# Optimization experiments

Hardware: AMD Instinct MI355X
Metric: run time of the kernel (lower is better)

## Reference

```python
import jax, jax.numpy as jnp
import numpy as np

K = 3
PAD = 1

def conv2d(x, w, b=None):
    # x: [B,C,H,W], w: [O,C,kh,kw], stride 1, padding 1
    y = jax.lax.conv_general_dilated(x, w, (1, 1), [(PAD, PAD), (PAD, PAD)],
                                     dimension_numbers=('NCHW', 'OIHW', 'NCHW'))
    if b is not None:
        y = y + b[None, :, None, None]
    return y

def deform_conv2d(x, offset, mask, w):
    # Faithful torchvision DeformConv2d (v2, stride=1, dilation=1, pad=1, no bias).
    # x: [B,C,H,W]; offset: [B,2*K*K,H,W] with (dy,dx) interleaved per kernel pt;
    # mask: [B,K*K,H,W]; w: [O,C,K,K]
    B, C, H, W = x.shape
    KK = K * K
    off = offset.reshape(B, KK, 2, H, W)
    offs_y, offs_x = off[:, :, 0], off[:, :, 1]           # [B,KK,H,W]
    ky = (jnp.arange(KK) // K).astype(jnp.float32) - PAD   # kernel row offsets
    kx = (jnp.arange(KK) % K).astype(jnp.float32) - PAD    # kernel col offsets
    py = offs_y + jnp.arange(H, dtype=jnp.float32)[None, None, :, None] + ky[None, :, None, None]
    px = offs_x + jnp.arange(W, dtype=jnp.float32)[None, None, None, :] + kx[None, :, None, None]
    y0f = jnp.floor(py); x0f = jnp.floor(px)
    wy = py - y0f; wx = px - x0f                           # bilinear fractions
    y0 = y0f.astype(jnp.int32); x0 = x0f.astype(jnp.int32)
    xf = x.reshape(B, C, H * W)

    def corner(yi, xi):
        valid = ((yi >= 0) & (yi < H) & (xi >= 0) & (xi < W)).astype(x.dtype)
        idx = jnp.clip(yi, 0, H - 1) * W + jnp.clip(xi, 0, W - 1)   # [B,KK,H,W]
        g = jax.vmap(lambda img, ix: img[:, ix])(xf, idx.reshape(B, KK * H * W))
        return g.reshape(B, C, KK, H, W) * valid[:, None]

    one = jnp.asarray(1.0, x.dtype)
    samp = (corner(y0, x0)         * ((one - wy) * (one - wx))[:, None]
          + corner(y0, x0 + 1)     * ((one - wy) * wx)[:, None]
          + corner(y0 + 1, x0)     * (wy * (one - wx))[:, None]
          + corner(y0 + 1, x0 + 1) * (wy * wx)[:, None])       # [B,C,KK,H,W]
    if mask is not None:
        samp = samp * mask[:, None]
    O = w.shape[0]
    return jnp.einsum('bckhw,ock->bohw', samp, w.reshape(O, C, KK))

def setup_inputs() -> dict:
    key = jax.random.key(0)
    ks = jax.random.split(key, 7)
    B, C, O, H, W = 4, 64, 64, 128, 128
    x = jax.random.normal(ks[0], (B, C, H, W), jnp.float32)
    ele = jax.random.normal(ks[1], (B, 1, H, W), jnp.float32)
    offset_w = jax.random.normal(ks[2], (2 * K * K, 1, 3, 3), jnp.float32) * 0.1
    offset_b = jnp.zeros((2 * K * K,), jnp.float32)
    mask_w = jax.random.normal(ks[3], (K * K, C, 3, 3), jnp.float32) * (1.0 / np.sqrt(C * 9))
    mask_b = jnp.zeros((K * K,), jnp.float32)
    deform_w = jax.random.normal(ks[4], (O, C, K, K), jnp.float32) * (1.0 / np.sqrt(C * 9))
    return {"x": x, "ele": ele, "offset_w": offset_w, "offset_b": offset_b,
            "mask_w": mask_w, "mask_b": mask_b, "deform_w": deform_w}

def reference(x, ele, offset_w, offset_b, mask_w, mask_b, deform_w):
    offset = conv2d(ele, offset_w, offset_b)                 # [B,18,H,W]
    mask = jax.nn.sigmoid(conv2d(x, mask_w, mask_b))         # [B,9,H,W]
    out = deform_conv2d(x, offset, mask, deform_w)           # [B,O,H,W]
    return jax.nn.relu(out)
```

## Files before the change

kernel.cpp:

```cpp
#include <hip/hip_runtime.h>
#include <hip/hip_bf16.h>
#include <hip/hip_fp16.h>

typedef _Float16 half8 __attribute__((ext_vector_type(8)));
typedef _Float16 half2v __attribute__((ext_vector_type(2)));
typedef float f32x4 __attribute__((ext_vector_type(4)));

#define B_ 4
#define C_ 64
#define O_ 64
#define H_ 128
#define W_ 128
#define HT 8
#define WT 16
#define HALO 3
#define RS 14
#define CS 22

__device__ __forceinline__ unsigned pkh(float lo, float hi) {
  half2v v = {(_Float16)lo, (_Float16)hi};
  return __builtin_bit_cast(unsigned, v);
}

__global__ void build_frags(const float* __restrict__ dw,
                            const float* __restrict__ mw,
                            _Float16* __restrict__ wsb) {
  int t = blockIdx.x * 256 + threadIdx.x;
  if (t < 36864) {
    int j = t & 7, lane = (t >> 3) & 63, ot = (t >> 9) & 3, s = t >> 11;
    int kk = s >> 1, ch = s & 1;
    int o = ot * 16 + (lane & 15);
    int c = ch * 32 + ((lane >> 4) << 3) + j;
    wsb[t] = (_Float16)dw[(o * 64 + c) * 9 + kk];
  } else if (t < 46080) {
    int t2 = t - 36864;
    int j = t2 & 7, lane = (t2 >> 3) & 63, s = t2 >> 9;
    int km = lane & 15;
    int c = (s & 1) * 32 + ((lane >> 4) << 3) + j;
    int tap = s >> 1;
    float v = (km < 9) ? mw[(km * 64 + c) * 9 + tap] : 0.0f;
    wsb[t] = (_Float16)v;
  }
}

__global__ __launch_bounds__(512, 4)
void deform_main(const float* __restrict__ x,
                 const float* __restrict__ ele,
                 const float* __restrict__ ow,
                 const float* __restrict__ ob,
                 const float* __restrict__ mb,
                 const _Float16* __restrict__ wsb,
                 float* __restrict__ out) {
  __shared__ uint4 xs4[RS * CS * 9];
  __shared__ uint4 dynbuf4[1152];
  _Float16* offl = (_Float16*)dynbuf4;
  uint2* cwb = (uint2*)((char*)dynbuf4 + 4608);
  unsigned* crc = (unsigned*)((char*)dynbuf4 + 4608 + 9216);
  f32x4* redbuf = (f32x4*)dynbuf4;

  const int tid = threadIdx.x;
  const int lane = tid & 63;
  const int wv = tid >> 6;
  const int pcl = lane & 15;
  const int lq = lane >> 4;

  const int bid = blockIdx.x;
  const int d = ((bid & 7) << 6) + (bid >> 3);
  const int b = d >> 7;
  const int t7 = d & 127;
  const int r0 = (t7 >> 3) * HT;
  const int c0 = (t7 & 7) * WT;

  float ev[9];
  {
    int tl = tid & 127;
    int pr = tl >> 4, pc = tl & 15;
    int h = r0 + pr, w = c0 + pc;
#pragma unroll
    for (int ty = 0; ty < 3; ++ty)
#pragma unroll
      for (int tx = 0; tx < 3; ++tx) {
        int gy = h - 1 + ty, gx = w - 1 + tx;
        float v = 0.0f;
        if ((unsigned)gy < 128u && (unsigned)gx < 128u)
          v = ele[b * (H_ * W_) + (gy << 7) + gx];
        ev[ty * 3 + tx] = v;
      }
  }

  {
    _Float16* xsb = (_Float16*)xs4;
    const int c2 = tid >> 4;
    const int pl = tid & 15;
    const float* xb0 = x + b * (C_ * H_ * W_) + (2 * c2) * (H_ * W_);
    const float* xb1 = xb0 + (H_ * W_);

    float2 va[11], vb[11];
#pragma unroll
    for (int k = 0; k < 11; ++k) {
      int it = pl + k * 16;
      int live = it < 168;
      int itc = live ? it : 167;
      int row = (itc * 5462) >> 16;
      int pc2 = itc - row * 12;
      int gy = r0 - HALO + row;
      int gx = c0 - 4 + 2 * pc2;
      float2 a = {0.0f, 0.0f}, bv2 = {0.0f, 0.0f};
      if (live && (unsigned)gy < 128u && (unsigned)gx < 127u) {
        int gi = (gy << 7) + gx;
        a = *(const float2*)(xb0 + gi);
        bv2 = *(const float2*)(xb1 + gi);
      }
      va[k] = a;
      vb[k] = bv2;
    }
#pragma unroll
    for (int k = 0; k < 11; ++k) {
      int it = pl + k * 16;
      if (it < 168) {
        int row = (it * 5462) >> 16;
        int pc2 = it - row * 12;
        int p = row * CS + 2 * pc2 - 1;
        if (pc2 > 0) {
          half2v h0 = {(_Float16)va[k].x, (_Float16)vb[k].x};
          *(half2v*)(xsb + p * 72 + 2 * c2) = h0;
        }
        if (pc2 < 11) {
          half2v h1 = {(_Float16)va[k].y, (_Float16)vb[k].y};
          *(half2v*)(xsb + (p + 1) * 72 + 2 * c2) = h1;
        }
      }
    }
  }

  if (tid < 128) {
#pragma unroll
    for (int ci = 0; ci < 18; ++ci) {
      float a = ob[ci];
#pragma unroll
      for (int tap = 0; tap < 9; ++tap) a += ev[tap] * ow[ci * 9 + tap];
      offl[tid * 18 + ci] = (_Float16)a;
    }
  }
  __syncthreads();

  {
    const half8* wfm8 = ((const half8*)wsb) + 4608;
    f32x4 macc = {0.f, 0.f, 0.f, 0.f};
#pragma unroll
    for (int s = 0; s < 18; ++s) {
      const int tap = s >> 1;
      const int chalf = s & 1;
      const int ty = tap / 3, tx = tap - ty * 3;
      half8 aw = wfm8[s * 64 + lane];
      const int csl = chalf * 4 + lq;
      int rc = (wv + (HALO - 1) + ty) * CS + (pcl + (HALO - 1) + tx);
      half8 xv = *(const half8*)(xs4 + rc * 9 + csl);
      macc = __builtin_amdgcn_mfma_f32_16x16x32_f16(aw, xv, macc, 0, 0, 0);
    }
    const int px = wv * 16 + pcl;
    const int h = r0 + wv, w = c0 + pcl;
#pragma unroll
    for (int r = 0; r < 4; ++r) {
      int kk = lq * 4 + r;
      if (kk < 9) {
        float a = macc[r] + mb[kk];
        float m = 1.0f / (1.0f + __expf(-a));
        int ky = kk / 3 - 1;
        int kx = kk - (kk / 3) * 3 - 1;
        half2v o2 = *(const half2v*)&offl[px * 18 + kk * 2];
        float py = (float)(h + ky) + (float)o2[0];
        float pxx = (float)(w + kx) + (float)o2[1];
        float fy = floorf(py), fx = floorf(pxx);
        float wy = py - fy, wx = pxx - fx;
        int iy = (int)fy - r0 + HALO;
        int ix = (int)fx - c0 + HALO;
        int vy0 = (unsigned)iy < (unsigned)RS;
        int vy1 = (unsigned)(iy + 1) < (unsigned)RS;
        int vx0 = (unsigned)ix < (unsigned)CS;
        int vx1 = (unsigned)(ix + 1) < (unsigned)CS;
        int cy0 = min(max(iy, 0), RS - 1), cy1 = min(max(iy + 1, 0), RS - 1);
        int cx0 = min(max(ix, 0), CS - 1), cx1 = min(max(ix + 1, 0), CS - 1);
        float wy0 = 1.0f - wy, wx0 = 1.0f - wx;
        float a00 = wy0 * wx0 * m * (float)(vy0 & vx0);
        float a01 = wy0 * wx * m * (float)(vy0 & vx1);
        float a10 = wy * wx0 * m * (float)(vy1 & vx0);
        float a11 = wy * wx * m * (float)(vy1 & vx1);
        int rc00 = cy0 * CS + cx0;
        int drow = (cy1 - cy0) * CS;
        int dcol = cx1 - cx0;
        uint2 cv;
        cv.x = pkh(a00, a01);
        cv.y = pkh(a10, a11);
        cwb[px * 9 + kk] = cv;
        crc[px * 9 + kk] =
            (unsigned)rc00 | ((unsigned)drow << 16) | ((unsigned)dcol << 24);
      }
    }
  }
  __syncthreads();

  const half8* wf8 = (const half8*)wsb;
  const int pxg = wv & 3;
  const int kh = wv >> 2;
  f32x4 acc[2][4];
#pragma unroll
  for (int pt = 0; pt < 2; ++pt)
#pragma unroll
    for (int ot = 0; ot < 4; ++ot) {
      f32x4 z = {0.f, 0.f, 0.f, 0.f};
      acc[pt][ot] = z;
    }

  const int pxA = pxg * 32 + pcl;
  const int pxB = pxA + 16;

#pragma unroll
  for (int s = 0; s < 9; ++s) {
    const int sidx = kh * 9 + s;
    const int kk = sidx >> 1;
    const int ch = sidx & 1;
    const int csl = ch * 4 + lq;
    half8 t[2];
#pragma unroll
    for (int pt = 0; pt < 2; ++pt) {
      const int px = pt ? pxB : pxA;
      uint2 cv = cwb[px * 9 + kk];
      unsigned rv = crc[px * 9 + kk];
      int rc00 = rv & 0xFFFF;
      int drow = (rv >> 16) & 0xFF;
      int dcol = rv >> 24;
      int rc01 = rc00 + dcol;
      int rc10 = rc00 + drow;
      int rc11 = rc10 + dcol;
      half2v c01 = __builtin_bit_cast(half2v, cv.x);
      half2v c23 = __builtin_bit_cast(half2v, cv.y);
      _Float16 a00 = c01[0], a01 = c01[1], a10 = c23[0], a11 = c23[1];
      half8 a00s = {a00, a00, a00, a00, a00, a00, a00, a00};
      half8 a01s = {a01, a01, a01, a01, a01, a01, a01, a01};
      half8 a10s = {a10, a10, a10, a10, a10, a10, a10, a10};
      half8 a11s = {a11, a11, a11, a11, a11, a11, a11, a11};
      half8 v00 = *(const half8*)(xs4 + rc00 * 9 + csl);
      half8 v01 = *(const half8*)(xs4 + rc01 * 9 + csl);
      half8 v10 = *(const half8*)(xs4 + rc10 * 9 + csl);
      half8 v11 = *(const half8*)(xs4 + rc11 * 9 + csl);
      t[pt] = v00 * a00s + v01 * a01s + v10 * a10s + v11 * a11s;
    }
#pragma unroll
    for (int ot = 0; ot < 4; ++ot) {
      half8 bw = wf8[(sidx * 4 + ot) * 64 + lane];
      acc[0][ot] = __builtin_amdgcn_mfma_f32_16x16x32_f16(bw, t[0], acc[0][ot], 0, 0, 0);
      acc[1][ot] = __builtin_amdgcn_mfma_f32_16x16x32_f16(bw, t[1], acc[1][ot], 0, 0, 0);
    }
  }

  __syncthreads();

#pragma unroll
  for (int pt = 0; pt < 2; ++pt) {
    if (kh == 1) {
#pragma unroll
      for (int ot = 0; ot < 4; ++ot)
        redbuf[((pxg * 4 + ot) * 4 + lq) * 16 + pcl] = acc[pt][ot];
    }
    __syncthreads();
    if (kh == 0) {
      const int px = pt ? pxB : pxA;
      const int h = r0 + (px >> 4);
      const int w = c0 + pcl;
#pragma unroll
      for (int ot = 0; ot < 4; ++ot) {
        f32x4 other = redbuf[((pxg * 4 + ot) * 4 + lq) * 16 + pcl];
#pragma unroll
        for (int r = 0; r < 4; ++r) {
          int o = ot * 16 + lq * 4 + r;
          float v = fmaxf(acc[pt][ot][r] + other[r], 0.0f);
          out[((b * O_ + o) << 14) + (h << 7) + w] = v;
        }
      }
    }
    __syncthreads();
  }
}

extern "C" void kernel_launch(void* const* d_in, const int* in_sizes, int n_in,
                              void* d_out, int out_size, void* d_ws, size_t ws_size,
                              hipStream_t stream) {
  const float* x   = (const float*)d_in[0];
  const float* ele = (const float*)d_in[1];
  const float* ow  = (const float*)d_in[2];
  const float* ob  = (const float*)d_in[3];
  const float* mw  = (const float*)d_in[4];
  const float* mb  = (const float*)d_in[5];
  const float* dw  = (const float*)d_in[6];
  _Float16* wsb = (_Float16*)d_ws;

  build_frags<<<180, 256, 0, stream>>>(dw, mw, wsb);
  deform_main<<<512, 512, 0, stream>>>(x, ele, ow, ob, mb, wsb,
                                       (float*)d_out);
}
```

Measured before the change: 30.36 us.

## Double block size to 1024 threads and split deform work per wave

Launches 1024-thread blocks, so each wave handles one 16-pixel tile and one channel half instead of two tiles. The sampling-coefficient computation is split out of the mask MFMA stage into a separate pass spread over all threads, with the mask staged in shared memory. The final reduction becomes a symmetric exchange in which each wave of a pair writes half the output channels, reusing the x tile buffer. The aim is more waves to hide LDS and MFMA latency, at the cost of an extra barrier, tighter register limits from launch_bounds(1024,8), and fewer loads per thread in the x staging.

```diff
diff --git a/kernel.cpp b/kernel.cpp
--- a/kernel.cpp
+++ b/kernel.cpp
@@ -43,7 +43,7 @@
   }
 }
 
-__global__ __launch_bounds__(512, 4)
+__global__ __launch_bounds__(1024, 8)
 void deform_main(const float* __restrict__ x,
                  const float* __restrict__ ele,
                  const float* __restrict__ ow,
@@ -52,11 +52,12 @@
                  const _Float16* __restrict__ wsb,
                  float* __restrict__ out) {
   __shared__ uint4 xs4[RS * CS * 9];
-  __shared__ uint4 dynbuf4[1152];
+  __shared__ uint4 dynbuf4[1296];
   _Float16* offl = (_Float16*)dynbuf4;
-  uint2* cwb = (uint2*)((char*)dynbuf4 + 4608);
-  unsigned* crc = (unsigned*)((char*)dynbuf4 + 4608 + 9216);
-  f32x4* redbuf = (f32x4*)dynbuf4;
+  _Float16* maskl = (_Float16*)((char*)dynbuf4 + 4608);
+  uint2* cwb = (uint2*)((char*)dynbuf4 + 4608 + 2304);
+  unsigned* crc = (unsigned*)((char*)dynbuf4 + 4608 + 2304 + 9216);
+  f32x4* xbuf = (f32x4*)xs4;
 
   const int tid = threadIdx.x;
   const int lane = tid & 63;
@@ -72,9 +73,8 @@
   const int c0 = (t7 & 7) * WT;
 
   float ev[9];
-  {
-    int tl = tid & 127;
-    int pr = tl >> 4, pc = tl & 15;
+  if (tid < 128) {
+    int pr = tid >> 4, pc = tid & 15;
     int h = r0 + pr, w = c0 + pc;
 #pragma unroll
     for (int ty = 0; ty < 3; ++ty)
@@ -90,15 +90,16 @@
 
   {
     _Float16* xsb = (_Float16*)xs4;
-    const int c2 = tid >> 4;
+    const int c2 = (tid >> 4) & 31;
     const int pl = tid & 15;
+    const int half = tid >> 9;
     const float* xb0 = x + b * (C_ * H_ * W_) + (2 * c2) * (H_ * W_);
     const float* xb1 = xb0 + (H_ * W_);
 
-    float2 va[11], vb[11];
-#pragma unroll
-    for (int k = 0; k < 11; ++k) {
-      int it = pl + k * 16;
+    float2 va[6], vb[6];
+#pragma unroll
+    for (int k = 0; k < 6; ++k) {
+      int it = pl + (2 * k + half) * 16;
       int live = it < 168;
       int itc = live ? it : 167;
       int row = (itc * 5462) >> 16;
@@ -115,8 +116,8 @@
       vb[k] = bv2;
     }
 #pragma unroll
-    for (int k = 0; k < 11; ++k) {
-      int it = pl + k * 16;
+    for (int k = 0; k < 6; ++k) {
+      int it = pl + (2 * k + half) * 16;
       if (it < 168) {
         int row = (it * 5462) >> 16;
         int pc2 = it - row * 12;
@@ -144,7 +145,7 @@
   }
   __syncthreads();
 
-  {
+  if (wv < 8) {
     const half8* wfm8 = ((const half8*)wsb) + 4608;
     f32x4 macc = {0.f, 0.f, 0.f, 0.f};
 #pragma unroll
@@ -158,62 +159,67 @@
       half8 xv = *(const half8*)(xs4 + rc * 9 + csl);
       macc = __builtin_amdgcn_mfma_f32_16x16x32_f16(aw, xv, macc, 0, 0, 0);
     }
-    const int px = wv * 16 + pcl;
-    const int h = r0 + wv, w = c0 + pcl;
+    int px = wv * 16 + pcl;
 #pragma unroll
     for (int r = 0; r < 4; ++r) {
-      int kk = lq * 4 + r;
-      if (kk < 9) {
-        float a = macc[r] + mb[kk];
+      int km = lq * 4 + r;
+      if (km < 9) {
+        float a = macc[r] + mb[km];
         float m = 1.0f / (1.0f + __expf(-a));
-        int ky = kk / 3 - 1;
-        int kx = kk - (kk / 3) * 3 - 1;
-        half2v o2 = *(const half2v*)&offl[px * 18 + kk * 2];
-        float py = (float)(h + ky) + (float)o2[0];
-        float pxx = (float)(w + kx) + (float)o2[1];
-        float fy = floorf(py), fx = floorf(pxx);
-        float wy = py - fy, wx = pxx - fx;
-        int iy = (int)fy - r0 + HALO;
-        int ix = (int)fx - c0 + HALO;
-        int vy0 = (unsigned)iy < (unsigned)RS;
-        int vy1 = (unsigned)(iy + 1) < (unsigned)RS;
-        int vx0 = (unsigned)ix < (unsigned)CS;
-        int vx1 = (unsigned)(ix + 1) < (unsigned)CS;
-        int cy0 = min(max(iy, 0), RS - 1), cy1 = min(max(iy + 1, 0), RS - 1);
-        int cx0 = min(max(ix, 0), CS - 1), cx1 = min(max(ix + 1, 0), CS - 1);
-        float wy0 = 1.0f - wy, wx0 = 1.0f - wx;
-        float a00 = wy0 * wx0 * m * (float)(vy0 & vx0);
-        float a01 = wy0 * wx * m * (float)(vy0 & vx1);
-        float a10 = wy * wx0 * m * (float)(vy1 & vx0);
-        float a11 = wy * wx * m * (float)(vy1 & vx1);
-        int rc00 = cy0 * CS + cx0;
-        int drow = (cy1 - cy0) * CS;
-        int dcol = cx1 - cx0;
-        uint2 cv;
-        cv.x = pkh(a00, a01);
-        cv.y = pkh(a10, a11);
-        cwb[px * 9 + kk] = cv;
-        crc[px * 9 + kk] =
-            (unsigned)rc00 | ((unsigned)drow << 16) | ((unsigned)dcol << 24);
-      }
-    }
+        maskl[px * 9 + km] = (_Float16)m;
+      }
+    }
+  }
+  __syncthreads();
+
+  for (int it = tid; it < 128 * 9; it += 1024) {
+    int px = (it * 7282) >> 16;
+    int kk = it - px * 9;
+    int pr = px >> 4, pc = px & 15;
+    int h = r0 + pr, w = c0 + pc;
+    int ky = kk / 3 - 1;
+    int kx = kk - (kk / 3) * 3 - 1;
+    half2v o2 = *(const half2v*)&offl[px * 18 + kk * 2];
+    float m = (float)maskl[px * 9 + kk];
+    float py = (float)(h + ky) + (float)o2[0];
+    float pxx = (float)(w + kx) + (float)o2[1];
+    float fy = floorf(py), fx = floorf(pxx);
+    float wy = py - fy, wx = pxx - fx;
+    int iy = (int)fy - r0 + HALO;
+    int ix = (int)fx - c0 + HALO;
+    int vy0 = (unsigned)iy < (unsigned)RS;
+    int vy1 = (unsigned)(iy + 1) < (unsigned)RS;
+    int vx0 = (unsigned)ix < (unsigned)CS;
+    int vx1 = (unsigned)(ix + 1) < (unsigned)CS;
+    int cy0 = min(max(iy, 0), RS - 1), cy1 = min(max(iy + 1, 0), RS - 1);
+    int cx0 = min(max(ix, 0), CS - 1), cx1 = min(max(ix + 1, 0), CS - 1);
+    float wy0 = 1.0f - wy, wx0 = 1.0f - wx;
+    float a00 = wy0 * wx0 * m * (float)(vy0 & vx0);
+    float a01 = wy0 * wx * m * (float)(vy0 & vx1);
+    float a10 = wy * wx0 * m * (float)(vy1 & vx0);
+    float a11 = wy * wx * m * (float)(vy1 & vx1);
+    int rc00 = cy0 * CS + cx0;
+    int drow = (cy1 - cy0) * CS;
+    int dcol = cx1 - cx0;
+    uint2 cv;
+    cv.x = pkh(a00, a01);
+    cv.y = pkh(a10, a11);
+    cwb[it] = cv;
+    crc[it] = (unsigned)rc00 | ((unsigned)drow << 16) | ((unsigned)dcol << 24);
   }
   __syncthreads();
 
   const half8* wf8 = (const half8*)wsb;
-  const int pxg = wv & 3;
-  const int kh = wv >> 2;
-  f32x4 acc[2][4];
-#pragma unroll
-  for (int pt = 0; pt < 2; ++pt)
-#pragma unroll
-    for (int ot = 0; ot < 4; ++ot) {
-      f32x4 z = {0.f, 0.f, 0.f, 0.f};
-      acc[pt][ot] = z;
-    }
-
-  const int pxA = pxg * 32 + pcl;
-  const int pxB = pxA + 16;
+  const int pxg = wv >> 1;
+  const int kh = wv & 1;
+  f32x4 acc[4];
+#pragma unroll
+  for (int ot = 0; ot < 4; ++ot) {
+    f32x4 z = {0.f, 0.f, 0.f, 0.f};
+    acc[ot] = z;
+  }
+
+  const int px = pxg * 16 + pcl;
 
 #pragma unroll
   for (int s = 0; s < 9; ++s) {
@@ -221,65 +227,77 @@
     const int kk = sidx >> 1;
     const int ch = sidx & 1;
     const int csl = ch * 4 + lq;
-    half8 t[2];
-#pragma unroll
-    for (int pt = 0; pt < 2; ++pt) {
-      const int px = pt ? pxB : pxA;
-      uint2 cv = cwb[px * 9 + kk];
-      unsigned rv = crc[px * 9 + kk];
-      int rc00 = rv & 0xFFFF;
-      int drow = (rv >> 16) & 0xFF;
-      int dcol = rv >> 24;
-      int rc01 = rc00 + dcol;
-      int rc10 = rc00 + drow;
-      int rc11 = rc10 + dcol;
-      half2v c01 = __builtin_bit_cast(half2v, cv.x);
-      half2v c23 = __builtin_bit_cast(half2v, cv.y);
-      _Float16 a00 = c01[0], a01 = c01[1], a10 = c23[0], a11 = c23[1];
-      half8 a00s = {a00, a00, a00, a00, a00, a00, a00, a00};
-      half8 a01s = {a01, a01, a01, a01, a01, a01, a01, a01};
-      half8 a10s = {a10, a10, a10, a10, a10, a10, a10, a10};
-      half8 a11s = {a11, a11, a11, a11, a11, a11, a11, a11};
-      half8 v00 = *(const half8*)(xs4 + rc00 * 9 + csl);
-      half8 v01 = *(const half8*)(xs4 + rc01 * 9 + csl);
-      half8 v10 = *(const half8*)(xs4 + rc10 * 9 + csl);
-      half8 v11 = *(const half8*)(xs4 + rc11 * 9 + csl);
-      t[pt] = v00 * a00s + v01 * a01s + v10 * a10s + v11 * a11s;
-    }
+    uint2 cv = cwb[px * 9 + kk];
+    unsigned rv = crc[px * 9 + kk];
+    int rc00 = rv & 0xFFFF;
+    int drow = (rv >> 16) & 0xFF;
+    int dcol = rv >> 24;
+    int rc01 = rc00 + dcol;
+    int rc10 = rc00 + drow;
+    int rc11 = rc10 + dcol;
+    half2v c01 = __builtin_bit_cast(half2v, cv.x);
+    half2v c23 = __builtin_bit_cast(half2v, cv.y);
+    _Float16 a00 = c01[0], a01 = c01[1], a10 = c23[0], a11 = c23[1];
+    half8 a00s = {a00, a00, a00, a00, a00, a00, a00, a00};
+    half8 a01s = {a01, a01, a01, a01, a01, a01, a01, a01};
+    half8 a10s = {a10, a10, a10, a10, a10, a10, a10, a10};
+    half8 a11s = {a11, a11, a11, a11, a11, a11, a11, a11};
+    half8 v00 = *(const half8*)(xs4 + rc00 * 9 + csl);
+    half8 v01 = *(const half8*)(xs4 + rc01 * 9 + csl);
+    half8 v10 = *(const half8*)(xs4 + rc10 * 9 + csl);
+    half8 v11 = *(const half8*)(xs4 + rc11 * 9 + csl);
+    half8 t = v00 * a00s + v01 * a01s + v10 * a10s + v11 * a11s;
 #pragma unroll
     for (int ot = 0; ot < 4; ++ot) {
       half8 bw = wf8[(sidx * 4 + ot) * 64 + lane];
-      acc[0][ot] = __builtin_amdgcn_mfma_f32_16x16x32_f16(bw, t[0], acc[0][ot], 0, 0, 0);
-      acc[1][ot] = __builtin_amdgcn_mfma_f32_16x16x32_f16(bw, t[1], acc[1][ot], 0, 0, 0);
-    }
-  }
-
-  __syncthreads();
-
-#pragma unroll
-  for (int pt = 0; pt < 2; ++pt) {
-    if (kh == 1) {
-#pragma unroll
-      for (int ot = 0; ot < 4; ++ot)
-        redbuf[((pxg * 4 + ot) * 4 + lq) * 16 + pcl] = acc[pt][ot];
-    }
-    __syncthreads();
+      acc[ot] = __builtin_amdgcn_mfma_f32_16x16x32_f16(bw, t, acc[ot], 0, 0, 0);
+    }
+  }
+
+  __syncthreads();
+
+  if (kh == 0) {
+    xbuf[(wv * 2 + 0) * 64 + lane] = acc[2];
+    xbuf[(wv * 2 + 1) * 64 + lane] = acc[3];
+  } else {
+    xbuf[(wv * 2 + 0) * 64 + lane] = acc[0];
+    xbuf[(wv * 2 + 1) * 64 + lane] = acc[1];
+  }
+  __syncthreads();
+
+  {
+    const int pw = wv ^ 1;
+    const int h = r0 + pxg;
+    const int w = c0 + pcl;
+    f32x4 p0 = xbuf[(pw * 2 + 0) * 64 + lane];
+    f32x4 p1 = xbuf[(pw * 2 + 1) * 64 + lane];
     if (kh == 0) {
-      const int px = pt ? pxB : pxA;
-      const int h = r0 + (px >> 4);
-      const int w = c0 + pcl;
-#pragma unroll
-      for (int ot = 0; ot < 4; ++ot) {
-        f32x4 other = redbuf[((pxg * 4 + ot) * 4 + lq) * 16 + pcl];
-#pragma unroll
-        for (int r = 0; r < 4; ++r) {
-          int o = ot * 16 + lq * 4 + r;
-          float v = fmaxf(acc[pt][ot][r] + other[r], 0.0f);
-          out[((b * O_ + o) << 14) + (h << 7) + w] = v;
-        }
-      }
-    }
-    __syncthreads();
+#pragma unroll
+      for (int r = 0; r < 4; ++r) {
+        int o = 0 * 16 + lq * 4 + r;
+        float v = fmaxf(acc[0][r] + p0[r], 0.0f);
+        out[((b * O_ + o) << 14) + (h << 7) + w] = v;
+      }
+#pragma unroll
+      for (int r = 0; r < 4; ++r) {
+        int o = 1 * 16 + lq * 4 + r;
+        float v = fmaxf(acc[1][r] + p1[r], 0.0f);
+        out[((b * O_ + o) << 14) + (h << 7) + w] = v;
+      }
+    } else {
+#pragma unroll
+      for (int r = 0; r < 4; ++r) {
+        int o = 2 * 16 + lq * 4 + r;
+        float v = fmaxf(acc[2][r] + p0[r], 0.0f);
+        out[((b * O_ + o) << 14) + (h << 7) + w] = v;
+      }
+#pragma unroll
+      for (int r = 0; r < 4; ++r) {
+        int o = 3 * 16 + lq * 4 + r;
+        float v = fmaxf(acc[3][r] + p1[r], 0.0f);
+        out[((b * O_ + o) << 14) + (h << 7) + w] = v;
+      }
+    }
   }
 }
 
@@ -296,6 +314,6 @@
   _Float16* wsb = (_Float16*)d_ws;
 
   build_frags<<<180, 256, 0, stream>>>(dw, mw, wsb);
-  deform_main<<<512, 512, 0, stream>>>(x, ele, ow, ob, mb, wsb,
-                                       (float*)d_out);
+  deform_main<<<512, 1024, 0, stream>>>(x, ele, ow, ob, mb, wsb,
+                                        (float*)d_out);
 }
```

After: 31.70 us. 1.04x slower.
